# Kernel tuning notes

Hardware: AMD Instinct MI355X
Metric: run time of the kernel (lower is better)

## Reference

```python
import jax, jax.numpy as jnp
import numpy as np

N_RAYS = 16384
MAX_STEPS = 512          # fixed march-step budget per ray (dense-padded packed samples)
GRID_R = 128             # occupancy grid resolution
NEAR = 0.05
FAR = 3.0
STEP = (FAR - NEAR) / MAX_STEPS   # render_step_size


def setup_inputs() -> dict:
    key = jax.random.key(0)
    k1, k2, k3 = jax.random.split(key, 3)
    rays_o = jax.random.uniform(k1, (N_RAYS, 3), minval=-0.5, maxval=0.5, dtype=jnp.float32)
    d = jax.random.normal(k2, (N_RAYS, 3), dtype=jnp.float32)
    rays_d = d / jnp.linalg.norm(d, axis=-1, keepdims=True)
    aabb = jnp.array([[-1.0, -1.0, -1.0], [1.0, 1.0, 1.0]], dtype=jnp.float32)
    occ_grid = jax.random.bernoulli(k3, 0.3, (GRID_R, GRID_R, GRID_R))  # bool occupancy
    return {"rays_o": rays_o, "rays_d": rays_d, "aabb": aabb, "occ_grid": occ_grid}


def reference(rays_o, rays_d, aabb, occ_grid):
    # --- ray / AABB intersection (per-ray valid t interval) ---
    safe_d = jnp.where(jnp.abs(rays_d) > 1e-10, rays_d, 1e-10)
    inv_d = 1.0 / safe_d
    t0 = (aabb[0] - rays_o) * inv_d          # [N,3]
    t1 = (aabb[1] - rays_o) * inv_d
    tmin = jnp.maximum(jnp.max(jnp.minimum(t0, t1), axis=-1), NEAR)   # [N]
    tmax = jnp.minimum(jnp.min(jnp.maximum(t0, t1), axis=-1), FAR)    # [N]

    # --- uniform marching bins (cone_angle = 0) ---
    edges = NEAR + jnp.arange(MAX_STEPS + 1, dtype=rays_o.dtype) * STEP
    starts = edges[:-1]                      # [S]
    ends = edges[1:]                         # [S]
    mids = 0.5 * (starts + ends)             # [S]

    # sample midpoint positions: [N,S,3]
    pos = rays_o[:, None, :] + rays_d[:, None, :] * mids[None, :, None]

    # --- occupancy-grid lookup (irregular gather) ---
    scale = (pos - aabb[0]) / (aabb[1] - aabb[0])          # [N,S,3] in [0,1) if inside
    idx = jnp.clip((scale * GRID_R).astype(jnp.int32), 0, GRID_R - 1)
    occ = occ_grid[idx[..., 0], idx[..., 1], idx[..., 2]]  # [N,S] bool
    inside = jnp.all((scale >= 0.0) & (scale < 1.0), axis=-1)

    valid = (starts[None, :] >= tmin[:, None]) & (ends[None, :] <= tmax[:, None]) & occ & inside  # [N,S]

    # --- packed_info (exclusive cumsum of per-ray counts) ---
    counts = valid.sum(axis=1).astype(jnp.int32)            # [N]
    offsets = jnp.concatenate([jnp.zeros((1,), jnp.int32), jnp.cumsum(counts)[:-1].astype(jnp.int32)])
    packed_info = jnp.stack([offsets, counts], axis=1)      # [N,2]

    # --- unpack_info equivalent: per-sample ray index, then irregular gather ---
    ray_indices = jnp.broadcast_to(jnp.arange(N_RAYS, dtype=jnp.int32)[:, None],
                                   (N_RAYS, MAX_STEPS)).reshape(-1)  # [N*S]
    mask = valid.reshape(-1)                                 # [N*S]
    maskf = mask.astype(rays_o.dtype)[:, None]

    origins = rays_o[ray_indices] * maskf                    # [N*S,3]
    dirs = rays_d[ray_indices] * maskf                       # [N*S,3]
    s_flat = jnp.where(mask, jnp.broadcast_to(starts, (N_RAYS, MAX_STEPS)).reshape(-1), 0.0)
    e_flat = jnp.where(mask, jnp.broadcast_to(ends, (N_RAYS, MAX_STEPS)).reshape(-1), 0.0)

    return origins, dirs, s_flat, e_flat, packed_info, ray_indices, mask
```

## Files before the change

### kernel.cpp

```cpp
#include <hip/hip_runtime.h>

#define N_RAYS 16384
#define MAX_STEPS 512
#define GRID_R 128
#define N_CELLS (GRID_R * GRID_R * GRID_R)
#define NS (N_RAYS * MAX_STEPS)

#define WS_COUNTS_OFF 1024
#define WS_BITS_OFF 131072
#define WS_NEEDED (WS_BITS_OFF + N_CELLS / 8)

__global__ void detect_dtype(const void* __restrict__ occ, int* __restrict__ flag) {
    __shared__ int ok_int, ok_flt;
    if (threadIdx.x == 0) { ok_int = 1; ok_flt = 1; }
    __syncthreads();
    const int*   pi = (const int*)occ;
    const float* pf = (const float*)occ;
    for (int i = threadIdx.x; i < 1024; i += blockDim.x) {
        int v = pi[i];
        if (v != 0 && v != 1) atomicAnd(&ok_int, 0);
        float f = pf[i];
        if (!(f == 0.0f || f == 1.0f)) atomicAnd(&ok_flt, 0);
    }
    __syncthreads();
    if (threadIdx.x == 0) flag[0] = ok_int ? 0 : (ok_flt ? 1 : 2);
}

__global__ __launch_bounds__(256)
void pack_occ(const void* __restrict__ occ, const int* __restrict__ flag_p,
              unsigned long long* __restrict__ bits) {
    const int mode = flag_p[0];
    const int idx = blockIdx.x * 256 + threadIdx.x;
    bool v;
    if (mode == 0)      v = ((const int*)occ)[idx] != 0;
    else if (mode == 1) v = ((const float*)occ)[idx] != 0.0f;
    else                v = ((const unsigned char*)occ)[idx] != 0;
    const unsigned long long b = __ballot(v);
    if ((threadIdx.x & 63) == 0) bits[idx >> 6] = b;
}

__global__ __launch_bounds__(512)
void sample_kernel(const float* __restrict__ rays_o, const float* __restrict__ rays_d,
                   const float* __restrict__ aabb, const void* __restrict__ occ,
                   const int* __restrict__ flag_p,
                   const unsigned int* __restrict__ bits, int use_bits,
                   float* __restrict__ out, int* __restrict__ counts)
{
    const int r = blockIdx.x;
    const int s = threadIdx.x;

    const float ox = rays_o[3 * r + 0], oy = rays_o[3 * r + 1], oz = rays_o[3 * r + 2];
    const float dx = rays_d[3 * r + 0], dy = rays_d[3 * r + 1], dz = rays_d[3 * r + 2];
    const float a0x = aabb[0], a0y = aabb[1], a0z = aabb[2];
    const float a1x = aabb[3], a1y = aabb[4], a1z = aabb[5];

    const float sdx = (fabsf(dx) > 1e-10f) ? dx : 1e-10f;
    const float sdy = (fabsf(dy) > 1e-10f) ? dy : 1e-10f;
    const float sdz = (fabsf(dz) > 1e-10f) ? dz : 1e-10f;
    const float invx = __fdiv_rn(1.0f, sdx);
    const float invy = __fdiv_rn(1.0f, sdy);
    const float invz = __fdiv_rn(1.0f, sdz);

    const float t0x = __fmul_rn(__fsub_rn(a0x, ox), invx);
    const float t1x = __fmul_rn(__fsub_rn(a1x, ox), invx);
    const float t0y = __fmul_rn(__fsub_rn(a0y, oy), invy);
    const float t1y = __fmul_rn(__fsub_rn(a1y, oy), invy);
    const float t0z = __fmul_rn(__fsub_rn(a0z, oz), invz);
    const float t1z = __fmul_rn(__fsub_rn(a1z, oz), invz);

    const float tmin = fmaxf(fmaxf(fmaxf(fminf(t0x, t1x), fminf(t0y, t1y)), fminf(t0z, t1z)), 0.05f);
    const float tmax = fminf(fminf(fminf(fmaxf(t0x, t1x), fmaxf(t0y, t1y)), fmaxf(t0z, t1z)), 3.0f);

    const float step_f = (float)((3.0 - 0.05) / 512.0);
    const float start = __fadd_rn(0.05f, __fmul_rn((float)s, step_f));
    const float end   = __fadd_rn(0.05f, __fmul_rn((float)(s + 1), step_f));
    const float mid   = __fmul_rn(0.5f, __fadd_rn(start, end));

    const float px = __fadd_rn(ox, __fmul_rn(dx, mid));
    const float py = __fadd_rn(oy, __fmul_rn(dy, mid));
    const float pz = __fadd_rn(oz, __fmul_rn(dz, mid));

    const float scx = __fdiv_rn(__fsub_rn(px, a0x), __fsub_rn(a1x, a0x));
    const float scy = __fdiv_rn(__fsub_rn(py, a0y), __fsub_rn(a1y, a0y));
    const float scz = __fdiv_rn(__fsub_rn(pz, a0z), __fsub_rn(a1z, a0z));

    const bool inside = (scx >= 0.0f) && (scx < 1.0f) &&
                        (scy >= 0.0f) && (scy < 1.0f) &&
                        (scz >= 0.0f) && (scz < 1.0f);
    const bool geom = inside && (start >= tmin) && (end <= tmax);

    bool valid = false;
    if (geom) {
        int gx = (int)__fmul_rn(scx, (float)GRID_R);
        int gy = (int)__fmul_rn(scy, (float)GRID_R);
        int gz = (int)__fmul_rn(scz, (float)GRID_R);
        gx = min(max(gx, 0), GRID_R - 1);
        gy = min(max(gy, 0), GRID_R - 1);
        gz = min(max(gz, 0), GRID_R - 1);
        const int lin = (gx * GRID_R + gy) * GRID_R + gz;
        if (use_bits) {
            valid = (bits[lin >> 5] >> (lin & 31)) & 1u;
        } else {
            const int mode = flag_p[0];
            if (mode == 0)      valid = ((const int*)occ)[lin] != 0;
            else if (mode == 1) valid = ((const float*)occ)[lin] != 0.0f;
            else                valid = ((const unsigned char*)occ)[lin] != 0;
        }
    }

    __shared__ float lmask[512];
    __shared__ int wcount[8];
    lmask[s] = valid ? 1.0f : 0.0f;
    const unsigned long long b = __ballot(valid);
    if ((s & 63) == 0) wcount[s >> 6] = __popcll(b);
    __syncthreads();

    if (s < 384) {
        const int f = 4 * s;
        float4 vo, vd;
#pragma unroll
        for (int k = 0; k < 4; ++k) {
            const int ff = f + k;
            const int smp = ff / 3;
            const int c = ff - smp * 3;
            const float m = lmask[smp];
            const float oc = (c == 0) ? ox : ((c == 1) ? oy : oz);
            const float dc = (c == 0) ? dx : ((c == 1) ? dy : dz);
            ((float*)&vo)[k] = __fmul_rn(m, oc);
            ((float*)&vd)[k] = __fmul_rn(m, dc);
        }
        ((float4*)out)[(long)r * 384 + s] = vo;
        ((float4*)(out + 3L * NS))[(long)r * 384 + s] = vd;
    }

    {
        const int grp = s >> 7;
        const int t = s & 127;
        float4 v;
#pragma unroll
        for (int k = 0; k < 4; ++k) {
            const int smp = 4 * t + k;
            const float m = lmask[smp];
            float val;
            if (grp == 0)      val = __fmul_rn(m, __fadd_rn(0.05f, __fmul_rn((float)smp, step_f)));
            else if (grp == 1) val = __fmul_rn(m, __fadd_rn(0.05f, __fmul_rn((float)(smp + 1), step_f)));
            else if (grp == 2) val = (float)r;
            else               val = m;
            ((float*)&v)[k] = val;
        }
        float* basep;
        if (grp == 0)      basep = out + 6L * NS;
        else if (grp == 1) basep = out + 7L * NS;
        else if (grp == 2) basep = out + 8L * NS + 2L * N_RAYS;
        else               basep = out + 8L * NS + 2L * N_RAYS + (long)NS;
        ((float4*)basep)[(long)r * 128 + t] = v;
    }

    if (s == 0) {
        int t = 0;
#pragma unroll
        for (int w = 0; w < 8; ++w) t += wcount[w];
        counts[r] = t;
    }
}

__global__ __launch_bounds__(1024)
void scan_kernel(const int* __restrict__ counts, float* __restrict__ packed)
{
    __shared__ int partial[1024];
    const int tid = threadIdx.x;
    const int base = tid * 16;
    int sum = 0;
#pragma unroll
    for (int i = 0; i < 16; ++i) sum += counts[base + i];
    partial[tid] = sum;
    __syncthreads();
    for (int off = 1; off < 1024; off <<= 1) {
        int v = (tid >= off) ? partial[tid - off] : 0;
        __syncthreads();
        partial[tid] += v;
        __syncthreads();
    }
    int run = (tid == 0) ? 0 : partial[tid - 1];
#pragma unroll
    for (int i = 0; i < 16; ++i) {
        const int c = counts[base + i];
        packed[2 * (base + i) + 0] = (float)run;
        packed[2 * (base + i) + 1] = (float)c;
        run += c;
    }
}

extern "C" void kernel_launch(void* const* d_in, const int* in_sizes, int n_in,
                              void* d_out, int out_size, void* d_ws, size_t ws_size,
                              hipStream_t stream) {
    const float* rays_o = (const float*)d_in[0];
    const float* rays_d = (const float*)d_in[1];
    const float* aabb   = (const float*)d_in[2];
    const void*  occ    = d_in[3];
    float* out = (float*)d_out;

    int* flag   = (int*)d_ws;
    int* counts = (int*)((char*)d_ws + WS_COUNTS_OFF);
    unsigned long long* bits64 = (unsigned long long*)((char*)d_ws + WS_BITS_OFF);
    const int use_bits = (ws_size >= (size_t)WS_NEEDED) ? 1 : 0;

    detect_dtype<<<1, 256, 0, stream>>>(occ, flag);
    if (use_bits)
        pack_occ<<<N_CELLS / 256, 256, 0, stream>>>(occ, flag, bits64);
    sample_kernel<<<N_RAYS, 512, 0, stream>>>(rays_o, rays_d, aabb, occ, flag,
                                              (const unsigned int*)bits64, use_bits,
                                              out, counts);
    scan_kernel<<<1, 1024, 0, stream>>>(counts, out + 8L * NS);
}
```

Before: 353.9 us.

## Fuse dtype detection into packing and scan into sampler via last-block ticket

Dtype detection now runs redundantly inside every pack_occ block, which removes a separate launch. The prefix scan over per-ray counts moves into the sample kernel: the last block to finish, found with an atomic ticket counter, performs the scan. Output stores become nontemporal vector stores to avoid polluting the cache. This adds a memset, atomics and a serial scan tail on one block, and it reads the first 4KB of occ in every pack block.

Result: slower. 1.276 ms (+260.7%).

```diff
diff --git a/kernel.cpp b/kernel.cpp
--- a/kernel.cpp
+++ b/kernel.cpp
@@ -6,34 +6,37 @@
 #define N_CELLS (GRID_R * GRID_R * GRID_R)
 #define NS (N_RAYS * MAX_STEPS)
 
+typedef float vfloat4 __attribute__((ext_vector_type(4)));
+
 #define WS_COUNTS_OFF 1024
 #define WS_BITS_OFF 131072
 #define WS_NEEDED (WS_BITS_OFF + N_CELLS / 8)
 
-__global__ void detect_dtype(const void* __restrict__ occ, int* __restrict__ flag) {
-    __shared__ int ok_int, ok_flt;
-    if (threadIdx.x == 0) { ok_int = 1; ok_flt = 1; }
-    __syncthreads();
-    const int*   pi = (const int*)occ;
+__global__ __launch_bounds__(256)
+void pack_occ(const void* __restrict__ occ, unsigned long long* __restrict__ bits) {
+    const int* pi = (const int*)occ;
     const float* pf = (const float*)occ;
-    for (int i = threadIdx.x; i < 1024; i += blockDim.x) {
-        int v = pi[i];
-        if (v != 0 && v != 1) atomicAnd(&ok_int, 0);
-        float f = pf[i];
-        if (!(f == 0.0f || f == 1.0f)) atomicAnd(&ok_flt, 0);
-    }
-    __syncthreads();
-    if (threadIdx.x == 0) flag[0] = ok_int ? 0 : (ok_flt ? 1 : 2);
-}
-
-__global__ __launch_bounds__(256)
-void pack_occ(const void* __restrict__ occ, const int* __restrict__ flag_p,
-              unsigned long long* __restrict__ bits) {
-    const int mode = flag_p[0];
+    bool oki = true, okf = true;
+#pragma unroll
+    for (int k = 0; k < 4; ++k) {
+        const int w = threadIdx.x * 4 + k;
+        const int v = pi[w];
+        oki = oki && (v == 0 || v == 1);
+        const float f = pf[w];
+        okf = okf && (f == 0.0f || f == 1.0f);
+    }
+    oki = __all(oki); okf = __all(okf);
+    __shared__ int s_oki[4], s_okf[4];
+    if ((threadIdx.x & 63) == 0) { s_oki[threadIdx.x >> 6] = oki; s_okf[threadIdx.x >> 6] = okf; }
+    __syncthreads();
+    const bool all_i = s_oki[0] && s_oki[1] && s_oki[2] && s_oki[3];
+    const bool all_f = s_okf[0] && s_okf[1] && s_okf[2] && s_okf[3];
+    const int mode = all_i ? 0 : (all_f ? 1 : 2);
+
     const int idx = blockIdx.x * 256 + threadIdx.x;
     bool v;
-    if (mode == 0)      v = ((const int*)occ)[idx] != 0;
-    else if (mode == 1) v = ((const float*)occ)[idx] != 0.0f;
+    if (mode == 0)      v = pi[idx] != 0;
+    else if (mode == 1) v = pf[idx] != 0.0f;
     else                v = ((const unsigned char*)occ)[idx] != 0;
     const unsigned long long b = __ballot(v);
     if ((threadIdx.x & 63) == 0) bits[idx >> 6] = b;
@@ -41,10 +44,9 @@
 
 __global__ __launch_bounds__(512)
 void sample_kernel(const float* __restrict__ rays_o, const float* __restrict__ rays_d,
-                   const float* __restrict__ aabb, const void* __restrict__ occ,
-                   const int* __restrict__ flag_p,
-                   const unsigned int* __restrict__ bits, int use_bits,
-                   float* __restrict__ out, int* __restrict__ counts)
+                   const float* __restrict__ aabb,
+                   const unsigned int* __restrict__ bits,
+                   float* __restrict__ out, int* counts, unsigned int* ticket)
 {
     const int r = blockIdx.x;
     const int s = threadIdx.x;
@@ -98,18 +100,12 @@
         gy = min(max(gy, 0), GRID_R - 1);
         gz = min(max(gz, 0), GRID_R - 1);
         const int lin = (gx * GRID_R + gy) * GRID_R + gz;
-        if (use_bits) {
-            valid = (bits[lin >> 5] >> (lin & 31)) & 1u;
-        } else {
-            const int mode = flag_p[0];
-            if (mode == 0)      valid = ((const int*)occ)[lin] != 0;
-            else if (mode == 1) valid = ((const float*)occ)[lin] != 0.0f;
-            else                valid = ((const unsigned char*)occ)[lin] != 0;
-        }
+        valid = (bits[lin >> 5] >> (lin & 31)) & 1u;
     }
 
     __shared__ float lmask[512];
     __shared__ int wcount[8];
+    __shared__ int s_last;
     lmask[s] = valid ? 1.0f : 0.0f;
     const unsigned long long b = __ballot(valid);
     if ((s & 63) == 0) wcount[s >> 6] = __popcll(b);
@@ -117,7 +113,7 @@
 
     if (s < 384) {
         const int f = 4 * s;
-        float4 vo, vd;
+        vfloat4 vo, vd;
 #pragma unroll
         for (int k = 0; k < 4; ++k) {
             const int ff = f + k;
@@ -126,17 +122,17 @@
             const float m = lmask[smp];
             const float oc = (c == 0) ? ox : ((c == 1) ? oy : oz);
             const float dc = (c == 0) ? dx : ((c == 1) ? dy : dz);
-            ((float*)&vo)[k] = __fmul_rn(m, oc);
-            ((float*)&vd)[k] = __fmul_rn(m, dc);
+            vo[k] = __fmul_rn(m, oc);
+            vd[k] = __fmul_rn(m, dc);
         }
-        ((float4*)out)[(long)r * 384 + s] = vo;
-        ((float4*)(out + 3L * NS))[(long)r * 384 + s] = vd;
+        __builtin_nontemporal_store(vo, (vfloat4*)out + (long)r * 384 + s);
+        __builtin_nontemporal_store(vd, (vfloat4*)(out + 3L * NS) + (long)r * 384 + s);
     }
 
     {
         const int grp = s >> 7;
         const int t = s & 127;
-        float4 v;
+        vfloat4 v;
 #pragma unroll
         for (int k = 0; k < 4; ++k) {
             const int smp = 4 * t + k;
@@ -146,17 +142,144 @@
             else if (grp == 1) val = __fmul_rn(m, __fadd_rn(0.05f, __fmul_rn((float)(smp + 1), step_f)));
             else if (grp == 2) val = (float)r;
             else               val = m;
-            ((float*)&v)[k] = val;
+            v[k] = val;
         }
         float* basep;
         if (grp == 0)      basep = out + 6L * NS;
         else if (grp == 1) basep = out + 7L * NS;
         else if (grp == 2) basep = out + 8L * NS + 2L * N_RAYS;
         else               basep = out + 8L * NS + 2L * N_RAYS + (long)NS;
-        ((float4*)basep)[(long)r * 128 + t] = v;
+        __builtin_nontemporal_store(v, (vfloat4*)basep + (long)r * 128 + t);
     }
 
     if (s == 0) {
+        int t = 0;
+#pragma unroll
+        for (int w = 0; w < 8; ++w) t += wcount[w];
+        __hip_atomic_store(&counts[r], t, __ATOMIC_RELEASE, __HIP_MEMORY_SCOPE_AGENT);
+        const unsigned int prev =
+            __hip_atomic_fetch_add(ticket, 1u, __ATOMIC_ACQ_REL, __HIP_MEMORY_SCOPE_AGENT);
+        s_last = (prev == (unsigned int)(N_RAYS - 1)) ? 1 : 0;
+    }
+    __syncthreads();
+
+    if (s_last) {
+        float* packed = out + 8L * NS;
+        __shared__ int partial[512];
+        const int base = s * 32;
+        int sum = 0;
+        for (int i = 0; i < 32; ++i)
+            sum += __hip_atomic_load(&counts[base + i], __ATOMIC_RELAXED, __HIP_MEMORY_SCOPE_AGENT);
+        partial[s] = sum;
+        __syncthreads();
+        for (int off = 1; off < 512; off <<= 1) {
+            const int v = (s >= off) ? partial[s - off] : 0;
+            __syncthreads();
+            partial[s] += v;
+            __syncthreads();
+        }
+        int run = (s == 0) ? 0 : partial[s - 1];
+        for (int i = 0; i < 32; ++i) {
+            const int c = __hip_atomic_load(&counts[base + i], __ATOMIC_RELAXED, __HIP_MEMORY_SCOPE_AGENT);
+            packed[2 * (base + i) + 0] = (float)run;
+            packed[2 * (base + i) + 1] = (float)c;
+            run += c;
+        }
+    }
+}
+
+__global__ void detect_dtype(const void* __restrict__ occ, int* __restrict__ flag) {
+    __shared__ int ok_int, ok_flt;
+    if (threadIdx.x == 0) { ok_int = 1; ok_flt = 1; }
+    __syncthreads();
+    const int*   pi = (const int*)occ;
+    const float* pf = (const float*)occ;
+    for (int i = threadIdx.x; i < 1024; i += blockDim.x) {
+        int v = pi[i];
+        if (v != 0 && v != 1) atomicAnd(&ok_int, 0);
+        float f = pf[i];
+        if (!(f == 0.0f || f == 1.0f)) atomicAnd(&ok_flt, 0);
+    }
+    __syncthreads();
+    if (threadIdx.x == 0) flag[0] = ok_int ? 0 : (ok_flt ? 1 : 2);
+}
+
+__global__ __launch_bounds__(512)
+void sample_fallback(const float* __restrict__ rays_o, const float* __restrict__ rays_d,
+                     const float* __restrict__ aabb, const void* __restrict__ occ,
+                     const int* __restrict__ flag_p, float* __restrict__ out,
+                     int* __restrict__ counts)
+{
+    const int r = blockIdx.x;
+    const int s = threadIdx.x;
+    const int mode = flag_p[0];
+    const float ox = rays_o[3 * r + 0], oy = rays_o[3 * r + 1], oz = rays_o[3 * r + 2];
+    const float dx = rays_d[3 * r + 0], dy = rays_d[3 * r + 1], dz = rays_d[3 * r + 2];
+    const float a0x = aabb[0], a0y = aabb[1], a0z = aabb[2];
+    const float a1x = aabb[3], a1y = aabb[4], a1z = aabb[5];
+    const float sdx = (fabsf(dx) > 1e-10f) ? dx : 1e-10f;
+    const float sdy = (fabsf(dy) > 1e-10f) ? dy : 1e-10f;
+    const float sdz = (fabsf(dz) > 1e-10f) ? dz : 1e-10f;
+    const float invx = __fdiv_rn(1.0f, sdx);
+    const float invy = __fdiv_rn(1.0f, sdy);
+    const float invz = __fdiv_rn(1.0f, sdz);
+    const float t0x = __fmul_rn(__fsub_rn(a0x, ox), invx);
+    const float t1x = __fmul_rn(__fsub_rn(a1x, ox), invx);
+    const float t0y = __fmul_rn(__fsub_rn(a0y, oy), invy);
+    const float t1y = __fmul_rn(__fsub_rn(a1y, oy), invy);
+    const float t0z = __fmul_rn(__fsub_rn(a0z, oz), invz);
+    const float t1z = __fmul_rn(__fsub_rn(a1z, oz), invz);
+    const float tmin = fmaxf(fmaxf(fmaxf(fminf(t0x, t1x), fminf(t0y, t1y)), fminf(t0z, t1z)), 0.05f);
+    const float tmax = fminf(fminf(fminf(fmaxf(t0x, t1x), fmaxf(t0y, t1y)), fmaxf(t0z, t1z)), 3.0f);
+    const float step_f = (float)((3.0 - 0.05) / 512.0);
+    const float start = __fadd_rn(0.05f, __fmul_rn((float)s, step_f));
+    const float end   = __fadd_rn(0.05f, __fmul_rn((float)(s + 1), step_f));
+    const float mid   = __fmul_rn(0.5f, __fadd_rn(start, end));
+    const float px = __fadd_rn(ox, __fmul_rn(dx, mid));
+    const float py = __fadd_rn(oy, __fmul_rn(dy, mid));
+    const float pz = __fadd_rn(oz, __fmul_rn(dz, mid));
+    const float scx = __fdiv_rn(__fsub_rn(px, a0x), __fsub_rn(a1x, a0x));
+    const float scy = __fdiv_rn(__fsub_rn(py, a0y), __fsub_rn(a1y, a0y));
+    const float scz = __fdiv_rn(__fsub_rn(pz, a0z), __fsub_rn(a1z, a0z));
+    const bool inside = (scx >= 0.0f) && (scx < 1.0f) &&
+                        (scy >= 0.0f) && (scy < 1.0f) &&
+                        (scz >= 0.0f) && (scz < 1.0f);
+    const bool geom = inside && (start >= tmin) && (end <= tmax);
+    bool valid = false;
+    if (geom) {
+        int gx = (int)__fmul_rn(scx, (float)GRID_R);
+        int gy = (int)__fmul_rn(scy, (float)GRID_R);
+        int gz = (int)__fmul_rn(scz, (float)GRID_R);
+        gx = min(max(gx, 0), GRID_R - 1);
+        gy = min(max(gy, 0), GRID_R - 1);
+        gz = min(max(gz, 0), GRID_R - 1);
+        const int lin = (gx * GRID_R + gy) * GRID_R + gz;
+        if (mode == 0)      valid = ((const int*)occ)[lin] != 0;
+        else if (mode == 1) valid = ((const float*)occ)[lin] != 0.0f;
+        else                valid = ((const unsigned char*)occ)[lin] != 0;
+    }
+    const int i = (r << 9) | s;
+    float* og = out;
+    float* dr = out + 3L * NS;
+    float* sf = out + 6L * NS;
+    float* ef = out + 7L * NS;
+    float* ri = out + 8L * NS + 2L * N_RAYS;
+    float* mk = ri + (long)NS;
+    og[3 * i + 0] = valid ? ox : 0.0f;
+    og[3 * i + 1] = valid ? oy : 0.0f;
+    og[3 * i + 2] = valid ? oz : 0.0f;
+    dr[3 * i + 0] = valid ? dx : 0.0f;
+    dr[3 * i + 1] = valid ? dy : 0.0f;
+    dr[3 * i + 2] = valid ? dz : 0.0f;
+    sf[i] = valid ? start : 0.0f;
+    ef[i] = valid ? end : 0.0f;
+    ri[i] = (float)r;
+    mk[i] = valid ? 1.0f : 0.0f;
+    const unsigned long long b = __ballot(valid);
+    __shared__ int wcount[8];
+    if ((threadIdx.x & 63) == 0) wcount[threadIdx.x >> 6] = __popcll(b);
+    __syncthreads();
+    if (threadIdx.x == 0) {
         int t = 0;
 #pragma unroll
         for (int w = 0; w < 8; ++w) t += wcount[w];
@@ -200,16 +323,20 @@
     const void*  occ    = d_in[3];
     float* out = (float*)d_out;
 
-    int* flag   = (int*)d_ws;
+    unsigned int* ticket = (unsigned int*)d_ws;
     int* counts = (int*)((char*)d_ws + WS_COUNTS_OFF);
-    unsigned long long* bits64 = (unsigned long long*)((char*)d_ws + WS_BITS_OFF);
-    const int use_bits = (ws_size >= (size_t)WS_NEEDED) ? 1 : 0;
-
-    detect_dtype<<<1, 256, 0, stream>>>(occ, flag);
-    if (use_bits)
-        pack_occ<<<N_CELLS / 256, 256, 0, stream>>>(occ, flag, bits64);
-    sample_kernel<<<N_RAYS, 512, 0, stream>>>(rays_o, rays_d, aabb, occ, flag,
-                                              (const unsigned int*)bits64, use_bits,
-                                              out, counts);
-    scan_kernel<<<1, 1024, 0, stream>>>(counts, out + 8L * NS);
-}
+
+    if (ws_size >= (size_t)WS_NEEDED) {
+        unsigned long long* bits64 = (unsigned long long*)((char*)d_ws + WS_BITS_OFF);
+        (void)hipMemsetAsync(ticket, 0, sizeof(unsigned int), stream);
+        pack_occ<<<N_CELLS / 256, 256, 0, stream>>>(occ, bits64);
+        sample_kernel<<<N_RAYS, 512, 0, stream>>>(rays_o, rays_d, aabb,
+                                                  (const unsigned int*)bits64,
+                                                  out, counts, ticket);
+    } else {
+        int* flag = (int*)d_ws;
+        detect_dtype<<<1, 256, 0, stream>>>(occ, flag);
+        sample_fallback<<<N_RAYS, 512, 0, stream>>>(rays_o, rays_d, aabb, occ, flag, out, counts);
+        scan_kernel<<<1, 1024, 0, stream>>>(counts, out + 8L * NS);
+    }
+}
```
